# Performance work log

Measured on AMD Instinct MI355X. Metric: run time of the kernel, lower is better.

## Reference

```python
import jax, jax.numpy as jnp
import numpy as np

N_NODES = 50000
N_EDGES = 300000
HID = 256
IN_S, IN_D, IN_E, OUT = 10, 12, 3, 3
K = 2


def _mlp(x, W1, b1, W2, b2):
    # 2-layer MLP: Linear -> relu -> Linear (mlp_layers=2, activation='relu')
    h = jax.nn.relu(x @ W1 + b1)
    return h @ W2 + b2


def setup_inputs() -> dict:
    key = jax.random.key(0)
    ks = jax.random.split(key, 16)

    def w(k, shape):
        return (jax.random.normal(k, shape, jnp.float32) * 0.05)

    z = lambda n: jnp.zeros((n,), jnp.float32)
    return {
        "static_features": jax.random.normal(ks[0], (N_NODES, IN_S), jnp.float32),
        "dynamic_features": jax.random.normal(ks[1], (N_NODES, IN_D), jnp.float32),
        "edge_index": jax.random.randint(ks[2], (2, N_EDGES), 0, N_NODES),
        "edge_attr": jax.random.normal(ks[3], (N_EDGES, IN_E), jnp.float32),
        # static node encoder
        "sW1": w(ks[4], (IN_S, HID)), "sb1": z(HID), "sW2": w(ks[5], (HID, HID)), "sb2": z(HID),
        # dynamic node encoder
        "dW1": w(ks[6], (IN_D, HID)), "db1": z(HID), "dW2": w(ks[7], (HID, HID)), "db2": z(HID),
        # edge encoder (edge_mlp=True)
        "eW1": w(ks[8], (IN_E, HID)), "eb1": z(HID), "eW2": w(ks[9], (HID, HID)), "eb2": z(HID),
        # SWEGNN edge-weight MLP: input [e_ij, x_s_i, x_s_j] -> HID
        "gW1": w(ks[10], (3 * HID, HID)), "gb1": z(HID), "gW2": w(ks[11], (HID, HID)), "gb2": z(HID),
        # decoder
        "oW1": w(ks[12], (HID, HID)), "ob1": z(HID), "oW2": w(ks[13], (HID, OUT)), "ob2": z(OUT),
    }


def reference(static_features, dynamic_features, edge_index, edge_attr,
              sW1, sb1, sW2, sb2, dW1, db1, dW2, db2,
              eW1, eb1, eW2, eb2, gW1, gb1, gW2, gb2,
              oW1, ob1, oW2, ob2):
    # Encoders
    x_s = _mlp(static_features, sW1, sb1, sW2, sb2)   # [N, HID]
    x_d = _mlp(dynamic_features, dW1, db1, dW2, db2)  # [N, HID]
    e = _mlp(edge_attr, eW1, eb1, eW2, eb2)           # [E, HID]

    src, dst = edge_index[0], edge_index[1]

    # Edge-conditioned weights from edge feats + static embeddings of endpoints
    g_in = jnp.concatenate([e, x_s[src], x_s[dst]], axis=-1)  # [E, 3*HID]
    g = _mlp(g_in, gW1, gb1, gW2, gb2)                        # [E, HID]

    # Degree normalization (normalize=True)
    deg = jax.ops.segment_sum(jnp.ones((src.shape[0],), jnp.float32), dst,
                              num_segments=N_NODES)
    inv_deg = (1.0 / jnp.maximum(deg, 1.0))[:, None]  # [N, 1]

    # K hops of SWE message passing: m_ij = g_ij * (h_j - h_i)  (with_gradient=True)
    h = x_d
    for _ in range(K):
        m = g * (h[src] - h[dst])                                  # [E, HID]
        aggr = jax.ops.segment_sum(m, dst, num_segments=N_NODES)   # [N, HID]
        h = h + aggr * inv_deg                                     # residual update

    x = jnp.tanh(h)  # gnn_activation='tanh'
    return _mlp(x, oW1, ob1, oW2, ob2)  # [N, OUT]
```

## Files before the change

kernel.cpp:

```cpp
#include <hip/hip_runtime.h>
#include <hip/hip_bf16.h>

#define N_NODES 50000
#define N_EDGES 300000
#define HID 256
#define AS 264
#define A0S 40
#define TN 32

typedef unsigned int uint;
typedef unsigned short ushort;
typedef short bf16x8 __attribute__((ext_vector_type(8)));
typedef unsigned short u16x8 __attribute__((ext_vector_type(8)));
typedef float f32x4 __attribute__((ext_vector_type(4)));

__device__ __forceinline__ float bf2f(ushort u){ union{uint i; float f;} v; v.i=((uint)u)<<16; return v.f; }
__device__ __forceinline__ ushort f2bf(float f){ __hip_bfloat16 h=__float2bfloat16(f); return *reinterpret_cast<ushort*>(&h); }

__device__ __forceinline__ f32x4 mfma16(bf16x8 a, bf16x8 b, f32x4 c){
    return __builtin_amdgcn_mfma_f32_16x16x32_bf16(a, b, c, 0, 0, 0);
}

__device__ __forceinline__ void wave_gemm(const ushort* act, const ushort* __restrict__ WT,
                                          int n0, int lane, f32x4 acc[4][4])
{
    #pragma unroll
    for (int mi=0;mi<4;mi++)
        #pragma unroll
        for (int ni=0;ni<4;ni++) acc[mi][ni]=(f32x4){0.f,0.f,0.f,0.f};
    const int rA=lane&15, kg=(lane>>4)*8;
    #pragma unroll
    for (int kk=0;kk<8;kk++){
        const int ka=kk*32+kg;
        bf16x8 a[4], b[4];
        #pragma unroll
        for (int mi=0;mi<4;mi++) a[mi]=*(const bf16x8*)&act[(mi*16+rA)*AS+ka];
        #pragma unroll
        for (int ni=0;ni<4;ni++) b[ni]=*(const bf16x8*)&WT[(size_t)((n0+ni*16+rA)*HID+ka)];
        #pragma unroll
        for (int mi=0;mi<4;mi++)
            #pragma unroll
            for (int ni=0;ni<4;ni++)
                acc[mi][ni]=mfma16(a[mi], b[ni], acc[mi][ni]);
    }
}

__device__ __forceinline__ void store_c_to_act(ushort* act, const f32x4 acc[4][4],
                                               int colb, int hi, bool relu)
{
    #pragma unroll
    for (int mi=0;mi<4;mi++)
        #pragma unroll
        for (int ni=0;ni<4;ni++)
            #pragma unroll
            for (int r=0;r<4;r++){
                float v=acc[mi][ni][r];
                if (relu) v=fmaxf(v,0.f);
                act[(mi*16+hi*4+r)*AS + colb+ni*16]=f2bf(v);
            }
}

__global__ void combine_weights(const float* __restrict__ sW2, const float* __restrict__ sb2,
                                const float* __restrict__ eW2, const float* __restrict__ eb2,
                                const float* __restrict__ gW1, const float* __restrict__ gb1,
                                const float* __restrict__ dW2, const float* __restrict__ gW2,
                                const float* __restrict__ oW1,
                                const float* __restrict__ eW1, const float* __restrict__ eb1,
                                ushort* __restrict__ WT_A, ushort* __restrict__ WT_B, ushort* __restrict__ WT_E,
                                ushort* __restrict__ WT_d, ushort* __restrict__ WT_g, ushort* __restrict__ WT_o,
                                ushort* __restrict__ WT_e1,
                                float* __restrict__ bias_A, float* __restrict__ bias_B)
{
    const int j = threadIdx.x;
    const int i = blockIdx.x;
    const int m = blockIdx.y;
    if (m==6){
        if (i<32)
            WT_e1[j*32+i] = f2bf(i<3 ? eW1[i*HID+j] : (i==3 ? eb1[j] : 0.f));
        return;
    }
    if (m>=3){
        if (i<HID){
            const float* S = (m==3)? dW2 : (m==4)? gW2 : oW1;
            ushort* D      = (m==3)? WT_d : (m==4)? WT_g : WT_o;
            D[j*HID+i]=f2bf(S[i*HID+j]);
        }
        return;
    }
    const float* L  = (m==2)? eW2 : sW2;
    const float* R  = gW1 + (m==0 ? HID*HID : (m==1 ? 2*HID*HID : 0));
    if (i < HID){
        float acc=0.f;
        for (int k=0;k<HID;k++) acc += L[i*HID+k]*R[k*HID+j];
        (m==0?WT_A:(m==1?WT_B:WT_E))[j*HID+i] = f2bf(acc);
    } else if (m==0){
        float acc=gb1[j];
        for (int k=0;k<HID;k++) acc += sb2[k]*gW1[(HID+k)*HID+j];
        for (int k=0;k<HID;k++) acc += eb2[k]*gW1[k*HID+j];
        bias_A[j]=acc;
    } else if (m==1){
        float acc=0.f;
        for (int k=0;k<HID;k++) acc += sb2[k]*gW1[(2*HID+k)*HID+j];
        bias_B[j]=acc;
    }
}

__global__ __launch_bounds__(256) void node_encode_mfma(
    const float* __restrict__ sfeat, const float* __restrict__ dfeat,
    const float* __restrict__ sW1, const float* __restrict__ sb1,
    const float* __restrict__ dW1, const float* __restrict__ db1,
    const ushort* __restrict__ WT_d, const float* __restrict__ db2,
    const ushort* __restrict__ WT_A, const float* __restrict__ bias_A,
    const ushort* __restrict__ WT_B, const float* __restrict__ bias_B,
    ushort* __restrict__ gA, ushort* __restrict__ gB, ushort* __restrict__ h0)
{
    __shared__ ushort act[64*AS];
    __shared__ float fb[64*12];
    const int tid=threadIdx.x;
    const int n0blk=blockIdx.x*64;
    const int wv=tid>>6, lane=tid&63, n0=wv*64;
    const int colb=n0+(lane&15);

    for (int i=tid;i<64*10;i+=256){
        int n=i/10, k=i-n*10; int gn=n0blk+n;
        fb[n*10+k]=(gn<N_NODES)? sfeat[(size_t)gn*10+k]:0.f;
    }
    __syncthreads();
    {   const int j=tid;
        float w[10];
        #pragma unroll
        for (int k=0;k<10;k++) w[k]=sW1[k*HID+j];
        const float b=sb1[j];
        for (int n=0;n<64;n++){
            float a=b;
            #pragma unroll
            for (int k=0;k<10;k++) a+=fb[n*10+k]*w[k];
            act[n*AS+j]=f2bf(fmaxf(a,0.f));
        }
    }
    __syncthreads();
    f32x4 acc[4][4];
    {
        wave_gemm(act, WT_A, n0, lane, acc);
        #pragma unroll
        for (int mi=0;mi<4;mi++){
            #pragma unroll
            for (int ni=0;ni<4;ni++){
                const int col=colb+ni*16; const float bA=bias_A[col];
                #pragma unroll
                for (int r=0;r<4;r++){
                    int rr=mi*16+(lane>>4)*4+r; int gn=n0blk+rr;
                    if (gn<N_NODES) gA[(size_t)gn*HID+col]=f2bf(acc[mi][ni][r]+bA);
                }
            }
        }
    }
    {
        wave_gemm(act, WT_B, n0, lane, acc);
        #pragma unroll
        for (int mi=0;mi<4;mi++){
            #pragma unroll
            for (int ni=0;ni<4;ni++){
                const int col=colb+ni*16; const float bB=bias_B[col];
                #pragma unroll
                for (int r=0;r<4;r++){
                    int rr=mi*16+(lane>>4)*4+r; int gn=n0blk+rr;
                    if (gn<N_NODES) gB[(size_t)gn*HID+col]=f2bf(acc[mi][ni][r]+bB);
                }
            }
        }
    }
    __syncthreads();
    for (int i=tid;i<64*12;i+=256){
        int n=i/12, k=i-n*12; int gn=n0blk+n;
        fb[n*12+k]=(gn<N_NODES)? dfeat[(size_t)gn*12+k]:0.f;
    }
    __syncthreads();
    {   const int j=tid;
        float w[12];
        #pragma unroll
        for (int k=0;k<12;k++) w[k]=dW1[k*HID+j];
        const float b=db1[j];
        for (int n=0;n<64;n++){
            float a=b;
            #pragma unroll
            for (int k=0;k<12;k++) a+=fb[n*12+k]*w[k];
            act[n*AS+j]=f2bf(fmaxf(a,0.f));
        }
    }
    __syncthreads();
    {
        wave_gemm(act, WT_d, n0, lane, acc);
        #pragma unroll
        for (int mi=0;mi<4;mi++){
            #pragma unroll
            for (int ni=0;ni<4;ni++){
                const int col=colb+ni*16; const float bo=db2[col];
                #pragma unroll
                for (int r=0;r<4;r++){
                    int rr=mi*16+(lane>>4)*4+r; int gn=n0blk+rr;
                    if (gn<N_NODES) h0[(size_t)gn*HID+col]=f2bf(acc[mi][ni][r]+bo);
                }
            }
        }
    }
}

__global__ __launch_bounds__(256) void edge_encode_mfma(
    const float* __restrict__ eattr, const int* __restrict__ eidx,
    const int* __restrict__ csr_src, const int* __restrict__ csr_eid,
    const ushort* __restrict__ WT_e1,
    const ushort* __restrict__ WT_E,
    const ushort* __restrict__ WT_g2, const float* __restrict__ gb2,
    const ushort* __restrict__ gA, const ushort* __restrict__ gB,
    ushort* __restrict__ g_out)
{
    __shared__ ushort act[64*AS];
    __shared__ ushort A0[64*A0S];
    __shared__ int si[64], di[64], ei[64];
    const int tid=threadIdx.x;
    const int s0=blockIdx.x*64;
    const int wv=tid>>6, lane=tid&63, n0=wv*64;
    const int rA=lane&15, kg=(lane>>4)*8, hi=lane>>4;
    const int colb=n0+rA;

    if (tid<64){
        int s=s0+tid; bool v=s<N_EDGES;
        int eid=v? csr_eid[s]:0;
        si[tid]=v? csr_src[s]:0;
        di[tid]=v? eidx[N_EDGES+eid]:0;
        ei[tid]=eid;
    }
    __syncthreads();
    {
        const int n=tid>>2, k0=(tid&3)*8;
        const int eid=ei[n];
        u16x8 v;
        #pragma unroll
        for (int j=0;j<8;j++){
            const int k=k0+j;
            float f = (k<3)? eattr[(size_t)eid*3+k] : (k==3? 1.f : 0.f);
            v[j]=f2bf(f);
        }
        *(u16x8*)&A0[n*A0S+k0]=v;
    }
    __syncthreads();
    f32x4 acc[4][4];
    {
        #pragma unroll
        for (int mi=0;mi<4;mi++)
            #pragma unroll
            for (int ni=0;ni<4;ni++) acc[mi][ni]=(f32x4){0.f,0.f,0.f,0.f};
        bf16x8 a[4], b[4];
        #pragma unroll
        for (int mi=0;mi<4;mi++) a[mi]=*(const bf16x8*)&A0[(mi*16+rA)*A0S+kg];
        #pragma unroll
        for (int ni=0;ni<4;ni++) b[ni]=*(const bf16x8*)&WT_e1[(size_t)(n0+ni*16+rA)*32+kg];
        #pragma unroll
        for (int mi=0;mi<4;mi++)
            #pragma unroll
            for (int ni=0;ni<4;ni++)
                acc[mi][ni]=mfma16(a[mi], b[ni], acc[mi][ni]);
        store_c_to_act(act, acc, colb, hi, true);
    }
    __syncthreads();
    wave_gemm(act, WT_E, n0, lane, acc);
    __syncthreads();
    store_c_to_act(act, acc, colb, hi, false);
    __syncthreads();
    {
        const int n=tid>>2, cc=(tid&3)*64;
        const int s=si[n], d=di[n];
        #pragma unroll
        for (int j=0;j<8;j++){
            u16x8 av=*(u16x8*)&act[n*AS+cc+j*8];
            u16x8 ga=*(const u16x8*)&gA[(size_t)s*HID+cc+j*8];
            u16x8 gb=*(const u16x8*)&gB[(size_t)d*HID+cc+j*8];
            u16x8 o;
            #pragma unroll
            for (int q=0;q<8;q++)
                o[q]=f2bf(fmaxf(bf2f(av[q])+bf2f(ga[q])+bf2f(gb[q]),0.f));
            *(u16x8*)&act[n*AS+cc+j*8]=o;
        }
    }
    __syncthreads();
    wave_gemm(act, WT_g2, n0, lane, acc);
    {
        #pragma unroll
        for (int mi=0;mi<4;mi++){
            #pragma unroll
            for (int ni=0;ni<4;ni++){
                const int col=colb+ni*16; const float bg=gb2[col];
                #pragma unroll
                for (int r=0;r<4;r++){
                    const int rr=mi*16+hi*4+r;
                    if (s0+rr<N_EDGES)
                        g_out[(size_t)(s0+rr)*HID+col]=f2bf(acc[mi][ni][r]+bg);
                }
            }
        }
    }
}

__global__ void deg_count(const int* __restrict__ eidx, uint* __restrict__ deg){
    int e=blockIdx.x*blockDim.x+threadIdx.x;
    if (e<N_EDGES) atomicAdd(&deg[eidx[N_EDGES+e]],1u);
}

__global__ void scan_kernel(const uint* __restrict__ deg, uint* __restrict__ row_start){
    __shared__ uint wtot[16];
    __shared__ uint woff[17];
    __shared__ uint carry_s;
    const int tid=threadIdx.x, lane=tid&63, wid=tid>>6;
    if (tid==0) carry_s=0;
    __syncthreads();
    for (uint base=0; base<N_NODES; base+=1024){
        uint idx=base+tid;
        uint v=(idx<N_NODES)? deg[idx]:0u;
        uint s=v;
        #pragma unroll
        for (int d=1; d<64; d<<=1){
            uint t=__shfl_up(s,d,64);
            if (lane>=d) s+=t;
        }
        if (lane==63) wtot[wid]=s;
        __syncthreads();
        if (tid==0){ uint r=0; for (int i=0;i<16;i++){ woff[i]=r; r+=wtot[i]; } woff[16]=r; }
        __syncthreads();
        uint excl = carry_s + woff[wid] + s - v;
        if (idx<N_NODES) row_start[idx]=excl;
        __syncthreads();
        if (tid==0) carry_s += woff[16];
        __syncthreads();
    }
}

__global__ void csr_fill(const int* __restrict__ eidx, const uint* __restrict__ row_start,
                         uint* __restrict__ cursor, int* __restrict__ csr_src, int* __restrict__ csr_eid){
    int e=blockIdx.x*blockDim.x+threadIdx.x;
    if (e>=N_EDGES) return;
    int d=eidx[N_EDGES+e];
    uint pos=atomicAdd(&cursor[d],1u);
    uint s=row_start[d]+pos;
    csr_src[s]=eidx[e];
    csr_eid[s]=e;
}

__global__ __launch_bounds__(256) void hop_kernel(
    const ushort* __restrict__ h_in, ushort* __restrict__ h_out,
    const ushort* __restrict__ g, const int* __restrict__ csr_src,
    const uint* __restrict__ row_start, const uint* __restrict__ deg)
{
    const int gw=(blockIdx.x*blockDim.x+threadIdx.x)>>6;
    if (gw>=N_NODES) return;
    const int c0=(threadIdx.x&63)*4;
    ushort4 hd4=*(const ushort4*)&h_in[(size_t)gw*HID+c0];
    float4 hd; hd.x=bf2f(hd4.x); hd.y=bf2f(hd4.y); hd.z=bf2f(hd4.z); hd.w=bf2f(hd4.w);
    float4 acc=make_float4(0,0,0,0);
    const uint st=row_start[gw], len=deg[gw];
    for (uint u=0;u<len;u++){
        uint s=st+u;
        int sn=csr_src[s];
        ushort4 g4=*(const ushort4*)&g[(size_t)s*HID+c0];
        ushort4 hs4=*(const ushort4*)&h_in[(size_t)sn*HID+c0];
        acc.x += bf2f(g4.x)*(bf2f(hs4.x)-hd.x);
        acc.y += bf2f(g4.y)*(bf2f(hs4.y)-hd.y);
        acc.z += bf2f(g4.z)*(bf2f(hs4.z)-hd.z);
        acc.w += bf2f(g4.w)*(bf2f(hs4.w)-hd.w);
    }
    const float inv=1.f/fmaxf((float)len,1.f);
    ushort4 o; o.x=f2bf(hd.x+acc.x*inv); o.y=f2bf(hd.y+acc.y*inv);
               o.z=f2bf(hd.z+acc.z*inv); o.w=f2bf(hd.w+acc.w*inv);
    *(ushort4*)&h_out[(size_t)gw*HID+c0]=o;
}

__global__ __launch_bounds__(256) void decoder_mfma(
    const ushort* __restrict__ h, const ushort* __restrict__ WT_o,
    const float* __restrict__ ob1, const float* __restrict__ oW2, const float* __restrict__ ob2,
    float* __restrict__ out)
{
    __shared__ ushort act[64*AS];
    const int tid=threadIdx.x, n0blk=blockIdx.x*64;
    const int wv=tid>>6, lane=tid&63, n0=wv*64, colb=n0+(lane&15);
    {
        const int row=tid>>2, cc=(tid&3)*64;
        const int gn=n0blk+row;
        #pragma unroll
        for (int k=0;k<64;k+=8){
            u16x8 t;
            if (gn<N_NODES){
                u16x8 v=*(const u16x8*)&h[(size_t)gn*HID+cc+k];
                #pragma unroll
                for (int j=0;j<8;j++) t[j]=f2bf(tanhf(bf2f(v[j])));
            } else {
                #pragma unroll
                for (int j=0;j<8;j++) t[j]=0;
            }
            *(u16x8*)&act[row*AS+cc+k]=t;
        }
    }
    __syncthreads();
    f32x4 acc[4][4];
    wave_gemm(act, WT_o, n0, lane, acc);
    __syncthreads();
    #pragma unroll
    for (int mi=0;mi<4;mi++){
        #pragma unroll
        for (int ni=0;ni<4;ni++){
            const int col=colb+ni*16; const float b1=ob1[col];
            #pragma unroll
            for (int r=0;r<4;r++){
                const int rr=mi*16+(lane>>4)*4+r;
                act[rr*AS+col]=f2bf(fmaxf(acc[mi][ni][r]+b1,0.f));
            }
        }
    }
    __syncthreads();
    if (tid<192){
        const int n=tid/3, o=tid-n*3;
        float a=ob2[o];
        for (int k=0;k<HID;k++) a+=bf2f(act[n*AS+k])*oW2[k*3+o];
        const int gn=n0blk+n;
        if (gn<N_NODES) out[(size_t)gn*3+o]=a;
    }
}

extern "C" void kernel_launch(void* const* d_in, const int* in_sizes, int n_in,
                              void* d_out, int out_size, void* d_ws, size_t ws_size,
                              hipStream_t stream)
{
    (void)in_sizes; (void)n_in; (void)out_size;
    const float* sfeat=(const float*)d_in[0];
    const float* dfeat=(const float*)d_in[1];
    const int*   eidx =(const int*)  d_in[2];
    const float* eattr=(const float*)d_in[3];
    const float* sW1=(const float*)d_in[4];  const float* sb1=(const float*)d_in[5];
    const float* sW2=(const float*)d_in[6];  const float* sb2=(const float*)d_in[7];
    const float* dW1=(const float*)d_in[8];  const float* db1=(const float*)d_in[9];
    const float* dW2=(const float*)d_in[10]; const float* db2=(const float*)d_in[11];
    const float* eW1=(const float*)d_in[12]; const float* eb1=(const float*)d_in[13];
    const float* eW2=(const float*)d_in[14]; const float* eb2=(const float*)d_in[15];
    const float* gW1=(const float*)d_in[16]; const float* gb1=(const float*)d_in[17];
    const float* gW2=(const float*)d_in[18]; const float* gb2=(const float*)d_in[19];
    const float* oW1=(const float*)d_in[20]; const float* ob1=(const float*)d_in[21];
    const float* oW2=(const float*)d_in[22]; const float* ob2=(const float*)d_in[23];
    float* out=(float*)d_out;

    char* p=(char*)d_ws;
    size_t used=0;
    auto alloc=[&](size_t bytes)->char*{
        char* r=p+used; used += (bytes+255)&~(size_t)255; return r;
    };
    ushort* WT_A=(ushort*)alloc(HID*HID*2);
    ushort* WT_B=(ushort*)alloc(HID*HID*2);
    ushort* WT_E=(ushort*)alloc(HID*HID*2);
    ushort* WT_d=(ushort*)alloc(HID*HID*2);
    ushort* WT_g=(ushort*)alloc(HID*HID*2);
    ushort* WT_o=(ushort*)alloc(HID*HID*2);
    ushort* WT_e1=(ushort*)alloc(HID*32*2);
    float* bias_A=(float*)alloc(HID*4);
    float* bias_B=(float*)alloc(HID*4);
    ushort* gA=(ushort*)alloc((size_t)N_NODES*HID*2);
    ushort* gB=(ushort*)alloc((size_t)N_NODES*HID*2);
    ushort* g =(ushort*)alloc((size_t)N_EDGES*HID*2);
    ushort* h0=(ushort*)alloc((size_t)N_NODES*HID*2);
    uint* deg      =(uint*)alloc(N_NODES*4);
    uint* row_start=(uint*)alloc(N_NODES*4);
    uint* cursor   =(uint*)alloc(N_NODES*4);
    int* csr_src=(int*)alloc(N_EDGES*4);
    int* csr_eid=(int*)alloc(N_EDGES*4);
    ushort* h1=gA;

    if (used > ws_size) return;

    hipMemsetAsync(deg, 0, N_NODES*4, stream);
    hipMemsetAsync(cursor, 0, N_NODES*4, stream);

    combine_weights<<<dim3(HID+1,7),256,0,stream>>>(sW2,sb2,eW2,eb2,gW1,gb1,dW2,gW2,oW1,eW1,eb1,
                                                    WT_A,WT_B,WT_E,WT_d,WT_g,WT_o,WT_e1,bias_A,bias_B);
    node_encode_mfma<<<(N_NODES+63)/64,256,0,stream>>>(sfeat,dfeat,sW1,sb1,dW1,db1,WT_d,db2,WT_A,bias_A,WT_B,bias_B,gA,gB,h0);
    deg_count<<<(N_EDGES+255)/256,256,0,stream>>>(eidx,deg);
    scan_kernel<<<1,1024,0,stream>>>(deg,row_start);
    csr_fill<<<(N_EDGES+255)/256,256,0,stream>>>(eidx,row_start,cursor,csr_src,csr_eid);
    edge_encode_mfma<<<(N_EDGES+63)/64,256,0,stream>>>(eattr,eidx,csr_src,csr_eid,WT_e1,WT_E,WT_g,gb2,gA,gB,g);
    hop_kernel<<<N_NODES/4,256,0,stream>>>(h0,h1,g,csr_src,row_start,deg);
    hop_kernel<<<N_NODES/4,256,0,stream>>>(h1,h0,g,csr_src,row_start,deg);
    decoder_mfma<<<(N_NODES+63)/64,256,0,stream>>>(h0,WT_o,ob1,oW2,ob2,out);
}
```

Baseline: 593.4 us.

## Use MFMA for first encoder layers, prefetch gathers, reorder edge blocks, set wave priority

Replaces the scalar first-layer static and dynamic node encoders with bf16 MFMA matmuls, folding the bias into the weights through an appended ones column. In the edge encoder, the gA row for each edge is prefetched into registers early, and each lane handles its own edge row for the gB combine, which removes one barrier. Edge blocks are remapped with a stride-8 interleaved index. s_setprio is raised around the MFMA loops. Together these aim to cut FMA work, hide gather latency and improve cache locality, at the cost of bf16 rounding of raw inputs and more register pressure.

```diff
diff --git a/kernel.cpp b/kernel.cpp
--- a/kernel.cpp
+++ b/kernel.cpp
@@ -6,7 +6,6 @@
 #define HID 256
 #define AS 264
 #define A0S 40
-#define TN 32
 
 typedef unsigned int uint;
 typedef unsigned short ushort;
@@ -29,6 +28,7 @@
         #pragma unroll
         for (int ni=0;ni<4;ni++) acc[mi][ni]=(f32x4){0.f,0.f,0.f,0.f};
     const int rA=lane&15, kg=(lane>>4)*8;
+    __builtin_amdgcn_s_setprio(1);
     #pragma unroll
     for (int kk=0;kk<8;kk++){
         const int ka=kk*32+kg;
@@ -43,6 +43,25 @@
             for (int ni=0;ni<4;ni++)
                 acc[mi][ni]=mfma16(a[mi], b[ni], acc[mi][ni]);
     }
+    __builtin_amdgcn_s_setprio(0);
+}
+
+__device__ __forceinline__ void wave_gemm32(const ushort* A0, const ushort* __restrict__ WT32,
+                                            int n0, int lane, f32x4 acc[4][4])
+{
+    const int rA=lane&15, kg=(lane>>4)*8;
+    bf16x8 a[4], b[4];
+    #pragma unroll
+    for (int mi=0;mi<4;mi++) a[mi]=*(const bf16x8*)&A0[(mi*16+rA)*A0S+kg];
+    #pragma unroll
+    for (int ni=0;ni<4;ni++) b[ni]=*(const bf16x8*)&WT32[(size_t)(n0+ni*16+rA)*32+kg];
+    __builtin_amdgcn_s_setprio(1);
+    #pragma unroll
+    for (int mi=0;mi<4;mi++)
+        #pragma unroll
+        for (int ni=0;ni<4;ni++)
+            acc[mi][ni]=mfma16(a[mi], b[ni], (f32x4){0.f,0.f,0.f,0.f}), void(0);
+    __builtin_amdgcn_s_setprio(0);
 }
 
 __device__ __forceinline__ void store_c_to_act(ushort* act, const f32x4 acc[4][4],
@@ -66,19 +85,19 @@
                                 const float* __restrict__ dW2, const float* __restrict__ gW2,
                                 const float* __restrict__ oW1,
                                 const float* __restrict__ eW1, const float* __restrict__ eb1,
+                                const float* __restrict__ sW1, const float* __restrict__ sb1,
+                                const float* __restrict__ dW1, const float* __restrict__ db1,
                                 ushort* __restrict__ WT_A, ushort* __restrict__ WT_B, ushort* __restrict__ WT_E,
                                 ushort* __restrict__ WT_d, ushort* __restrict__ WT_g, ushort* __restrict__ WT_o,
-                                ushort* __restrict__ WT_e1,
+                                ushort* __restrict__ WT_e1, ushort* __restrict__ WT_s1, ushort* __restrict__ WT_d1,
                                 float* __restrict__ bias_A, float* __restrict__ bias_B)
 {
     const int j = threadIdx.x;
     const int i = blockIdx.x;
     const int m = blockIdx.y;
-    if (m==6){
-        if (i<32)
-            WT_e1[j*32+i] = f2bf(i<3 ? eW1[i*HID+j] : (i==3 ? eb1[j] : 0.f));
-        return;
-    }
+    if (m==6){ if (i<32) WT_e1[j*32+i] = f2bf(i<3 ? eW1[i*HID+j] : (i==3 ? eb1[j] : 0.f)); return; }
+    if (m==7){ if (i<32) WT_s1[j*32+i] = f2bf(i<10? sW1[i*HID+j] : (i==10? sb1[j] : 0.f)); return; }
+    if (m==8){ if (i<32) WT_d1[j*32+i] = f2bf(i<12? dW1[i*HID+j] : (i==12? db1[j] : 0.f)); return; }
     if (m>=3){
         if (i<HID){
             const float* S = (m==3)? dW2 : (m==4)? gW2 : oW1;
@@ -107,39 +126,60 @@
 
 __global__ __launch_bounds__(256) void node_encode_mfma(
     const float* __restrict__ sfeat, const float* __restrict__ dfeat,
-    const float* __restrict__ sW1, const float* __restrict__ sb1,
-    const float* __restrict__ dW1, const float* __restrict__ db1,
+    const ushort* __restrict__ WT_s1, const ushort* __restrict__ WT_d1,
     const ushort* __restrict__ WT_d, const float* __restrict__ db2,
     const ushort* __restrict__ WT_A, const float* __restrict__ bias_A,
     const ushort* __restrict__ WT_B, const float* __restrict__ bias_B,
     ushort* __restrict__ gA, ushort* __restrict__ gB, ushort* __restrict__ h0)
 {
     __shared__ ushort act[64*AS];
-    __shared__ float fb[64*12];
+    __shared__ ushort A0[64*A0S];
     const int tid=threadIdx.x;
     const int n0blk=blockIdx.x*64;
     const int wv=tid>>6, lane=tid&63, n0=wv*64;
-    const int colb=n0+(lane&15);
-
-    for (int i=tid;i<64*10;i+=256){
-        int n=i/10, k=i-n*10; int gn=n0blk+n;
-        fb[n*10+k]=(gn<N_NODES)? sfeat[(size_t)gn*10+k]:0.f;
-    }
-    __syncthreads();
-    {   const int j=tid;
-        float w[10];
-        #pragma unroll
-        for (int k=0;k<10;k++) w[k]=sW1[k*HID+j];
-        const float b=sb1[j];
-        for (int n=0;n<64;n++){
-            float a=b;
-            #pragma unroll
-            for (int k=0;k<10;k++) a+=fb[n*10+k]*w[k];
-            act[n*AS+j]=f2bf(fmaxf(a,0.f));
-        }
+    const int rA=lane&15, kg=(lane>>4)*8, hi=lane>>4;
+    const int colb=n0+rA;
+
+    {
+        const int n=tid>>2, k0=(tid&3)*8;
+        const int gn=n0blk+n;
+        u16x8 v;
+        #pragma unroll
+        for (int j=0;j<8;j++){
+            const int k=k0+j;
+            float f = (gn<N_NODES && k<10)? sfeat[(size_t)gn*10+k] : (k==10? 1.f : 0.f);
+            v[j]=f2bf(f);
+        }
+        *(u16x8*)&A0[n*A0S+k0]=v;
     }
     __syncthreads();
     f32x4 acc[4][4];
+    {
+        bf16x8 a[4], b[4];
+        #pragma unroll
+        for (int mi=0;mi<4;mi++) a[mi]=*(const bf16x8*)&A0[(mi*16+rA)*A0S+kg];
+        #pragma unroll
+        for (int ni=0;ni<4;ni++) b[ni]=*(const bf16x8*)&WT_s1[(size_t)(n0+ni*16+rA)*32+kg];
+        #pragma unroll
+        for (int mi=0;mi<4;mi++)
+            #pragma unroll
+            for (int ni=0;ni<4;ni++)
+                acc[mi][ni]=mfma16(a[mi], b[ni], (f32x4){0.f,0.f,0.f,0.f});
+        store_c_to_act(act, acc, colb, hi, true);
+    }
+    __syncthreads();
+    {
+        const int n=tid>>2, k0=(tid&3)*8;
+        const int gn=n0blk+n;
+        u16x8 v;
+        #pragma unroll
+        for (int j=0;j<8;j++){
+            const int k=k0+j;
+            float f = (gn<N_NODES && k<12)? dfeat[(size_t)gn*12+k] : (k==12? 1.f : 0.f);
+            v[j]=f2bf(f);
+        }
+        *(u16x8*)&A0[n*A0S+k0]=v;
+    }
     {
         wave_gemm(act, WT_A, n0, lane, acc);
         #pragma unroll
@@ -149,7 +189,7 @@
                 const int col=colb+ni*16; const float bA=bias_A[col];
                 #pragma unroll
                 for (int r=0;r<4;r++){
-                    int rr=mi*16+(lane>>4)*4+r; int gn=n0blk+rr;
+                    int rr=mi*16+hi*4+r; int gn=n0blk+rr;
                     if (gn<N_NODES) gA[(size_t)gn*HID+col]=f2bf(acc[mi][ni][r]+bA);
                 }
             }
@@ -164,29 +204,25 @@
                 const int col=colb+ni*16; const float bB=bias_B[col];
                 #pragma unroll
                 for (int r=0;r<4;r++){
-                    int rr=mi*16+(lane>>4)*4+r; int gn=n0blk+rr;
+                    int rr=mi*16+hi*4+r; int gn=n0blk+rr;
                     if (gn<N_NODES) gB[(size_t)gn*HID+col]=f2bf(acc[mi][ni][r]+bB);
                 }
             }
         }
     }
     __syncthreads();
-    for (int i=tid;i<64*12;i+=256){
-        int n=i/12, k=i-n*12; int gn=n0blk+n;
-        fb[n*12+k]=(gn<N_NODES)? dfeat[(size_t)gn*12+k]:0.f;
-    }
-    __syncthreads();
-    {   const int j=tid;
-        float w[12];
-        #pragma unroll
-        for (int k=0;k<12;k++) w[k]=dW1[k*HID+j];
-        const float b=db1[j];
-        for (int n=0;n<64;n++){
-            float a=b;
-            #pragma unroll
-            for (int k=0;k<12;k++) a+=fb[n*12+k]*w[k];
-            act[n*AS+j]=f2bf(fmaxf(a,0.f));
-        }
+    {
+        bf16x8 a[4], b[4];
+        #pragma unroll
+        for (int mi=0;mi<4;mi++) a[mi]=*(const bf16x8*)&A0[(mi*16+rA)*A0S+kg];
+        #pragma unroll
+        for (int ni=0;ni<4;ni++) b[ni]=*(const bf16x8*)&WT_d1[(size_t)(n0+ni*16+rA)*32+kg];
+        #pragma unroll
+        for (int mi=0;mi<4;mi++)
+            #pragma unroll
+            for (int ni=0;ni<4;ni++)
+                acc[mi][ni]=mfma16(a[mi], b[ni], (f32x4){0.f,0.f,0.f,0.f});
+        store_c_to_act(act, acc, colb, hi, true);
     }
     __syncthreads();
     {
@@ -198,7 +234,7 @@
                 const int col=colb+ni*16; const float bo=db2[col];
                 #pragma unroll
                 for (int r=0;r<4;r++){
-                    int rr=mi*16+(lane>>4)*4+r; int gn=n0blk+rr;
+                    int rr=mi*16+hi*4+r; int gn=n0blk+rr;
                     if (gn<N_NODES) h0[(size_t)gn*HID+col]=f2bf(acc[mi][ni][r]+bo);
                 }
             }
@@ -219,7 +255,8 @@
     __shared__ ushort A0[64*A0S];
     __shared__ int si[64], di[64], ei[64];
     const int tid=threadIdx.x;
-    const int s0=blockIdx.x*64;
+    const int bid=blockIdx.x;
+    const int s0=((bid&7)*586 + (bid>>3))*64;
     const int wv=tid>>6, lane=tid&63, n0=wv*64;
     const int rA=lane&15, kg=(lane>>4)*8, hi=lane>>4;
     const int colb=n0+rA;
@@ -232,6 +269,13 @@
         ei[tid]=eid;
     }
     __syncthreads();
+    u16x8 gpa[8];
+    {
+        const ushort* garow=&gA[(size_t)si[lane]*HID + n0];
+        #pragma unroll
+        for (int j=0;j<8;j++)
+            gpa[j]=*(const u16x8*)&garow[((j+lane)&7)*8];
+    }
     {
         const int n=tid>>2, k0=(tid&3)*8;
         const int eid=ei[n];
@@ -247,40 +291,35 @@
     __syncthreads();
     f32x4 acc[4][4];
     {
+        bf16x8 a[4], b[4];
+        #pragma unroll
+        for (int mi=0;mi<4;mi++) a[mi]=*(const bf16x8*)&A0[(mi*16+rA)*A0S+kg];
+        #pragma unroll
+        for (int ni=0;ni<4;ni++) b[ni]=*(const bf16x8*)&WT_e1[(size_t)(n0+ni*16+rA)*32+kg];
         #pragma unroll
         for (int mi=0;mi<4;mi++)
             #pragma unroll
-            for (int ni=0;ni<4;ni++) acc[mi][ni]=(f32x4){0.f,0.f,0.f,0.f};
-        bf16x8 a[4], b[4];
-        #pragma unroll
-        for (int mi=0;mi<4;mi++) a[mi]=*(const bf16x8*)&A0[(mi*16+rA)*A0S+kg];
-        #pragma unroll
-        for (int ni=0;ni<4;ni++) b[ni]=*(const bf16x8*)&WT_e1[(size_t)(n0+ni*16+rA)*32+kg];
-        #pragma unroll
-        for (int mi=0;mi<4;mi++)
-            #pragma unroll
             for (int ni=0;ni<4;ni++)
-                acc[mi][ni]=mfma16(a[mi], b[ni], acc[mi][ni]);
+                acc[mi][ni]=mfma16(a[mi], b[ni], (f32x4){0.f,0.f,0.f,0.f});
         store_c_to_act(act, acc, colb, hi, true);
     }
     __syncthreads();
     wave_gemm(act, WT_E, n0, lane, acc);
     __syncthreads();
     store_c_to_act(act, acc, colb, hi, false);
-    __syncthreads();
-    {
-        const int n=tid>>2, cc=(tid&3)*64;
-        const int s=si[n], d=di[n];
+    {
+        const ushort* gbrow=&gB[(size_t)di[lane]*HID + n0];
+        ushort* arow=&act[lane*AS + n0];
         #pragma unroll
         for (int j=0;j<8;j++){
-            u16x8 av=*(u16x8*)&act[n*AS+cc+j*8];
-            u16x8 ga=*(const u16x8*)&gA[(size_t)s*HID+cc+j*8];
-            u16x8 gb=*(const u16x8*)&gB[(size_t)d*HID+cc+j*8];
+            const int jb=((j+lane)&7)*8;
+            u16x8 av=*(u16x8*)&arow[jb];
+            u16x8 gb=*(const u16x8*)&gbrow[jb];
             u16x8 o;
             #pragma unroll
             for (int q=0;q<8;q++)
-                o[q]=f2bf(fmaxf(bf2f(av[q])+bf2f(ga[q])+bf2f(gb[q]),0.f));
-            *(u16x8*)&act[n*AS+cc+j*8]=o;
+                o[q]=f2bf(fmaxf(bf2f(av[q])+bf2f(gpa[j][q])+bf2f(gb[q]),0.f));
+            *(u16x8*)&arow[jb]=o;
         }
     }
     __syncthreads();
@@ -458,6 +497,8 @@
     ushort* WT_g=(ushort*)alloc(HID*HID*2);
     ushort* WT_o=(ushort*)alloc(HID*HID*2);
     ushort* WT_e1=(ushort*)alloc(HID*32*2);
+    ushort* WT_s1=(ushort*)alloc(HID*32*2);
+    ushort* WT_d1=(ushort*)alloc(HID*32*2);
     float* bias_A=(float*)alloc(HID*4);
     float* bias_B=(float*)alloc(HID*4);
     ushort* gA=(ushort*)alloc((size_t)N_NODES*HID*2);
@@ -476,9 +517,9 @@
     hipMemsetAsync(deg, 0, N_NODES*4, stream);
     hipMemsetAsync(cursor, 0, N_NODES*4, stream);
 
-    combine_weights<<<dim3(HID+1,7),256,0,stream>>>(sW2,sb2,eW2,eb2,gW1,gb1,dW2,gW2,oW1,eW1,eb1,
-                                                    WT_A,WT_B,WT_E,WT_d,WT_g,WT_o,WT_e1,bias_A,bias_B);
-    node_encode_mfma<<<(N_NODES+63)/64,256,0,stream>>>(sfeat,dfeat,sW1,sb1,dW1,db1,WT_d,db2,WT_A,bias_A,WT_B,bias_B,gA,gB,h0);
+    combine_weights<<<dim3(HID+1,9),256,0,stream>>>(sW2,sb2,eW2,eb2,gW1,gb1,dW2,gW2,oW1,eW1,eb1,sW1,sb1,dW1,db1,
+                                                    WT_A,WT_B,WT_E,WT_d,WT_g,WT_o,WT_e1,WT_s1,WT_d1,bias_A,bias_B);
+    node_encode_mfma<<<(N_NODES+63)/64,256,0,stream>>>(sfeat,dfeat,WT_s1,WT_d1,WT_d,db2,WT_A,bias_A,WT_B,bias_B,gA,gB,h0);
     deg_count<<<(N_EDGES+255)/256,256,0,stream>>>(eidx,deg);
     scan_kernel<<<1,1024,0,stream>>>(deg,row_start);
     csr_fill<<<(N_EDGES+255)/256,256,0,stream>>>(eidx,row_start,cursor,csr_src,csr_eid);
```

New measurement: 591.9 us. No clear change (-0.2%).
